# Kernel optimization log

Measured on AMD Instinct MI355X. Metric: run time of the kernel, lower is better.

The kernel has to match this reference:

```python
import jax, jax.numpy as jnp
import numpy as np

N = 4096
D_IN = 1024
D_OUT = 1024
NUM_HEADS = 16
HEAD_DIM = D_OUT // NUM_HEADS


def setup_inputs() -> dict:
    key = jax.random.key(0)
    ks = jax.random.split(key, 7)
    scale = 1.0 / np.sqrt(D_IN)
    return {
        "q": jax.random.normal(ks[0], (N, D_IN), dtype=jnp.float32),
        "k": jax.random.normal(ks[1], (N, D_IN), dtype=jnp.float32),
        "v": jax.random.normal(ks[2], (N, D_IN), dtype=jnp.float32),
        "W_q": jax.random.normal(ks[3], (D_IN, D_OUT), dtype=jnp.float32) * scale,
        "W_k": jax.random.normal(ks[4], (D_IN, D_OUT), dtype=jnp.float32) * scale,
        "W_v": jax.random.normal(ks[5], (D_IN, D_OUT), dtype=jnp.float32) * scale,
        "W_o": jax.random.normal(ks[6], (D_OUT, D_OUT), dtype=jnp.float32) * scale,
    }


def reference(q, k, v, W_q, W_k, W_v, W_o):
    n = q.shape[0]
    # QKV projections -> [h, n, d]
    Q = (q @ W_q).reshape(n, NUM_HEADS, HEAD_DIM).transpose(1, 0, 2)
    K = (k @ W_k).reshape(n, NUM_HEADS, HEAD_DIM).transpose(1, 0, 2)
    V = (v @ W_v).reshape(n, NUM_HEADS, HEAD_DIM).transpose(1, 0, 2)
    scores = jnp.einsum('hid,hjd->hij', Q, K) / jnp.sqrt(jnp.float32(HEAD_DIM))
    attn = jax.nn.softmax(scores, axis=-1)  # dropout p=0.0 (eval) -> no-op
    h = jnp.einsum('hij,hjd->hid', attn, V)
    h = h.transpose(1, 0, 2).reshape(n, D_OUT)
    return h @ W_o
```

## Files before the change

kernel.cpp:

```cpp
#include <hip/hip_runtime.h>
#include <math.h>

#define NTOK   4096
#define DMODEL 1024
#define NHEADS 16
#define HDIM   64
#define KDIM   1024

typedef __attribute__((ext_vector_type(8))) short          bf16x8;
typedef __attribute__((ext_vector_type(4))) float          f32x4;
typedef __attribute__((ext_vector_type(4))) unsigned short us4;

static __device__ __forceinline__ unsigned short f2bf(float f) {
    unsigned int u = __float_as_uint(f);
    u += 0x7fffu + ((u >> 16) & 1u);
    return (unsigned short)(u >> 16);
}

static __device__ __forceinline__ unsigned int pk2bf(float a, float b) {
#if __has_builtin(__builtin_amdgcn_cvt_pk_bf16_f32)
    return __builtin_bit_cast(unsigned int,
                              __builtin_amdgcn_cvt_pk_bf16_f32(a, b));
#else
    unsigned int ua = __float_as_uint(a) + 0x8000u;
    unsigned int ub = __float_as_uint(b) + 0x8000u;
    return __builtin_amdgcn_perm(ub, ua, 0x07060302u);
#endif
}

#if __has_builtin(__builtin_amdgcn_exp2f)
#define EXP2(x) __builtin_amdgcn_exp2f(x)
#else
#define EXP2(x) exp2f(x)
#endif

static __device__ __forceinline__ void async_copy16(void* lds, const void* g) {
    __builtin_amdgcn_global_load_lds(
        (const __attribute__((address_space(1))) unsigned int*)g,
        (__attribute__((address_space(3))) unsigned int*)lds, 16, 0, 0);
}

__global__ __launch_bounds__(256)
void cast_wt_kernel(const float* __restrict__ Wq, const float* __restrict__ Wk,
                    const float* __restrict__ Wv, const float* __restrict__ Wo,
                    unsigned short* __restrict__ Tq, unsigned short* __restrict__ Tk,
                    unsigned short* __restrict__ Tv, unsigned short* __restrict__ To) {
    __shared__ float Ws[64][65];
    const float* W;
    unsigned short* T;
    switch (blockIdx.z) {
        case 0:  W = Wq; T = Tq; break;
        case 1:  W = Wk; T = Tk; break;
        case 2:  W = Wv; T = Tv; break;
        default: W = Wo; T = To; break;
    }
    const int k0 = blockIdx.x * 64, n0 = blockIdx.y * 64;
    const int t = threadIdx.x;
    #pragma unroll
    for (int i = 0; i < 4; i++) {
        int c  = i * 256 + t;
        int kk = c >> 4;
        int n4 = (c & 15) << 2;
        *(float4*)(&Ws[kk][n4]) =
            *(const float4*)(W + (size_t)(k0 + kk) * DMODEL + n0 + n4);
    }
    __syncthreads();
    #pragma unroll
    for (int i = 0; i < 4; i++) {
        int c  = i * 256 + t;
        int nn = c >> 4;
        int k4 = (c & 15) << 2;
        us4 o = { f2bf(Ws[k4 + 0][nn]), f2bf(Ws[k4 + 1][nn]),
                  f2bf(Ws[k4 + 2][nn]), f2bf(Ws[k4 + 3][nn]) };
        *(us4*)(T + (size_t)(n0 + nn) * KDIM + k0 + k4) = o;
    }
}

__global__ __launch_bounds__(256)
void cast_in_kernel(const float* __restrict__ q, const float* __restrict__ k,
                    const float* __restrict__ v,
                    unsigned short* __restrict__ Qb,
                    unsigned short* __restrict__ Kb,
                    unsigned short* __restrict__ Vb) {
    const float* src;
    unsigned short* dst;
    switch (blockIdx.y) {
        case 0:  src = q; dst = Qb; break;
        case 1:  src = k; dst = Kb; break;
        default: src = v; dst = Vb; break;
    }
    size_t i = ((size_t)blockIdx.x * 256 + threadIdx.x) * 8;
    float4 f0 = *(const float4*)(src + i);
    float4 f1 = *(const float4*)(src + i + 4);
    uint2 o0 = { pk2bf(f0.x, f0.y), pk2bf(f0.z, f0.w) };
    uint2 o1 = { pk2bf(f1.x, f1.y), pk2bf(f1.z, f1.w) };
    *(uint2*)(dst + i)     = o0;
    *(uint2*)(dst + i + 4) = o1;
}

__global__ __launch_bounds__(256, 3)
void qkv_gemm_pre(const unsigned short* __restrict__ Qb,
                  const unsigned short* __restrict__ Kb,
                  const unsigned short* __restrict__ Vb,
                  const unsigned short* __restrict__ Btq,
                  const unsigned short* __restrict__ Btk,
                  const unsigned short* __restrict__ Btv,
                  unsigned short* __restrict__ Oq, unsigned short* __restrict__ Ok,
                  unsigned short* __restrict__ Ov) {
    __shared__ unsigned short As[128 * 64];
    __shared__ unsigned short Bs[128 * 64];

    const unsigned short* A;
    const unsigned short* Bt;
    unsigned short* Out;
    int mode;
    float sc;
    switch (blockIdx.z) {
        case 0:  A = Qb; Bt = Btq; Out = Oq; mode = 1; sc = 0.18033688011112042f; break;
        case 1:  A = Kb; Bt = Btk; Out = Ok; mode = 1; sc = 1.0f; break;
        default: A = Vb; Bt = Btv; Out = Ov; mode = 2; sc = 1.0f; break;
    }

    const int t    = threadIdx.x;
    const int w    = t >> 6;
    const int lane = t & 63;
    const int quad = lane >> 4;
    const int l15  = lane & 15;
    const int wr   = w >> 1, wc = w & 1;
    const int bm   = blockIdx.y * 128, bn = blockIdx.x * 128;

    f32x4 acc[4][4];
    #pragma unroll
    for (int i = 0; i < 4; i++)
        #pragma unroll
        for (int j = 0; j < 4; j++) acc[i][j] = (f32x4)(0.f);

    for (int k0 = 0; k0 < KDIM; k0 += 64) {
        __syncthreads();
        #pragma unroll
        for (int i = 0; i < 4; i++) {
            int cb = (i * 4 + w) * 64;
            int c  = cb + lane;
            int r  = c >> 3;
            int ko = (c & 7) * 8;
            async_copy16((void*)(Bs + cb * 8),
                         (const void*)(Bt + (size_t)(bn + r) * KDIM + k0 + ko));
            async_copy16((void*)(As + cb * 8),
                         (const void*)(A + (size_t)(bm + r) * KDIM + k0 + ko));
        }
        __syncthreads();
        #pragma unroll
        for (int kq = 0; kq < 2; kq++) {
            bf16x8 af[4], bf[4];
            #pragma unroll
            for (int mt = 0; mt < 4; mt++)
                af[mt] = *(bf16x8*)(As + (wr * 64 + mt * 16 + l15) * 64 + kq * 32 + quad * 8);
            #pragma unroll
            for (int nt = 0; nt < 4; nt++)
                bf[nt] = *(bf16x8*)(Bs + (wc * 64 + nt * 16 + l15) * 64 + kq * 32 + quad * 8);
            #pragma unroll
            for (int mt = 0; mt < 4; mt++)
                #pragma unroll
                for (int nt = 0; nt < 4; nt++)
                    acc[mt][nt] = __builtin_amdgcn_mfma_f32_16x16x32_bf16(
                        af[mt], bf[nt], acc[mt][nt], 0, 0, 0);
        }
    }

    #pragma unroll
    for (int mt = 0; mt < 4; mt++) {
        #pragma unroll
        for (int nt = 0; nt < 4; nt++) {
            int col  = bn + wc * 64 + nt * 16 + l15;
            int row0 = bm + wr * 64 + mt * 16 + quad * 4;
            if (mode == 1) {
                size_t base = ((size_t)(col >> 6)) * NTOK * HDIM + (col & 63);
                #pragma unroll
                for (int r = 0; r < 4; r++)
                    Out[base + (size_t)(row0 + r) * HDIM] = f2bf(acc[mt][nt][r] * sc);
            } else {
                size_t base = ((size_t)(col >> 6)) * HDIM * NTOK +
                              (size_t)(col & 63) * NTOK + row0;
                us4 o = { f2bf(acc[mt][nt][0]), f2bf(acc[mt][nt][1]),
                          f2bf(acc[mt][nt][2]), f2bf(acc[mt][nt][3]) };
                *(us4*)(Out + base) = o;
            }
        }
    }
}

__global__ __launch_bounds__(256, 3)
void qkv_gemm(const float* __restrict__ Aq, const float* __restrict__ Ak,
              const float* __restrict__ Av,
              const unsigned short* __restrict__ Btq,
              const unsigned short* __restrict__ Btk,
              const unsigned short* __restrict__ Btv,
              unsigned short* __restrict__ Oq, unsigned short* __restrict__ Ok,
              unsigned short* __restrict__ Ov) {
    __shared__ unsigned short As[128 * 64];
    __shared__ unsigned short Bs[128 * 64];

    const float* A;
    const unsigned short* Bt;
    unsigned short* Out;
    int mode;
    float sc;
    switch (blockIdx.z) {
        case 0:  A = Aq; Bt = Btq; Out = Oq; mode = 1; sc = 0.18033688011112042f; break;
        case 1:  A = Ak; Bt = Btk; Out = Ok; mode = 1; sc = 1.0f; break;
        default: A = Av; Bt = Btv; Out = Ov; mode = 2; sc = 1.0f; break;
    }

    const int t    = threadIdx.x;
    const int w    = t >> 6;
    const int lane = t & 63;
    const int quad = lane >> 4;
    const int l15  = lane & 15;
    const int wr   = w >> 1, wc = w & 1;
    const int bm   = blockIdx.y * 128, bn = blockIdx.x * 128;

    f32x4 acc[4][4];
    #pragma unroll
    for (int i = 0; i < 4; i++)
        #pragma unroll
        for (int j = 0; j < 4; j++) acc[i][j] = (f32x4)(0.f);

    for (int k0 = 0; k0 < KDIM; k0 += 64) {
        __syncthreads();
        #pragma unroll
        for (int i = 0; i < 4; i++) {
            int cb = (i * 4 + w) * 64;
            int c  = cb + lane;
            int r  = c >> 3;
            int ko = (c & 7) * 8;
            async_copy16((void*)(Bs + cb * 8),
                         (const void*)(Bt + (size_t)(bn + r) * KDIM + k0 + ko));
        }
        #pragma unroll
        for (int i = 0; i < 4; i++) {
            int c2 = i * 256 + t;
            int r  = c2 >> 3;
            int k8 = (c2 & 7) * 8;
            const float* src = A + (size_t)(bm + r) * KDIM + k0 + k8;
            float4 f0 = *(const float4*)(src);
            float4 f1 = *(const float4*)(src + 4);
            uint2 p0 = { pk2bf(f0.x, f0.y), pk2bf(f0.z, f0.w) };
            uint2 p1 = { pk2bf(f1.x, f1.y), pk2bf(f1.z, f1.w) };
            *(uint2*)(As + r * 64 + k8)     = p0;
            *(uint2*)(As + r * 64 + k8 + 4) = p1;
        }
        __syncthreads();
        #pragma unroll
        for (int kq = 0; kq < 2; kq++) {
            bf16x8 af[4], bf[4];
            #pragma unroll
            for (int mt = 0; mt < 4; mt++)
                af[mt] = *(bf16x8*)(As + (wr * 64 + mt * 16 + l15) * 64 + kq * 32 + quad * 8);
            #pragma unroll
            for (int nt = 0; nt < 4; nt++)
                bf[nt] = *(bf16x8*)(Bs + (wc * 64 + nt * 16 + l15) * 64 + kq * 32 + quad * 8);
            #pragma unroll
            for (int mt = 0; mt < 4; mt++)
                #pragma unroll
                for (int nt = 0; nt < 4; nt++)
                    acc[mt][nt] = __builtin_amdgcn_mfma_f32_16x16x32_bf16(
                        af[mt], bf[nt], acc[mt][nt], 0, 0, 0);
        }
    }

    #pragma unroll
    for (int mt = 0; mt < 4; mt++) {
        #pragma unroll
        for (int nt = 0; nt < 4; nt++) {
            int col  = bn + wc * 64 + nt * 16 + l15;
            int row0 = bm + wr * 64 + mt * 16 + quad * 4;
            if (mode == 1) {
                size_t base = ((size_t)(col >> 6)) * NTOK * HDIM + (col & 63);
                #pragma unroll
                for (int r = 0; r < 4; r++)
                    Out[base + (size_t)(row0 + r) * HDIM] = f2bf(acc[mt][nt][r] * sc);
            } else {
                size_t base = ((size_t)(col >> 6)) * HDIM * NTOK +
                              (size_t)(col & 63) * NTOK + row0;
                us4 o = { f2bf(acc[mt][nt][0]), f2bf(acc[mt][nt][1]),
                          f2bf(acc[mt][nt][2]), f2bf(acc[mt][nt][3]) };
                *(us4*)(Out + base) = o;
            }
        }
    }
}

__global__ __launch_bounds__(256, 3)
void out_gemm(const unsigned short* __restrict__ A,
              const unsigned short* __restrict__ Bt,
              float* __restrict__ Out) {
    __shared__ unsigned short As[64 * 64];
    __shared__ unsigned short Bs[128 * 64];

    const int t    = threadIdx.x;
    const int w    = t >> 6;
    const int lane = t & 63;
    const int quad = lane >> 4;
    const int l15  = lane & 15;
    const int wr   = w >> 1, wc = w & 1;
    const int bm   = blockIdx.y * 64, bn = blockIdx.x * 128;

    f32x4 acc[2][4];
    #pragma unroll
    for (int i = 0; i < 2; i++)
        #pragma unroll
        for (int j = 0; j < 4; j++) acc[i][j] = (f32x4)(0.f);

    for (int k0 = 0; k0 < KDIM; k0 += 64) {
        __syncthreads();
        #pragma unroll
        for (int i = 0; i < 4; i++) {
            int cb = (i * 4 + w) * 64;
            int c  = cb + lane;
            int r  = c >> 3;
            int ko = (c & 7) * 8;
            async_copy16((void*)(Bs + cb * 8),
                         (const void*)(Bt + (size_t)(bn + r) * KDIM + k0 + ko));
        }
        #pragma unroll
        for (int i = 0; i < 2; i++) {
            int cb = (i * 4 + w) * 64;
            int c  = cb + lane;
            int r  = c >> 3;
            int ko = (c & 7) * 8;
            async_copy16((void*)(As + cb * 8),
                         (const void*)(A + (size_t)(bm + r) * KDIM + k0 + ko));
        }
        __syncthreads();
        #pragma unroll
        for (int kq = 0; kq < 2; kq++) {
            bf16x8 af[2], bf[4];
            #pragma unroll
            for (int mt = 0; mt < 2; mt++)
                af[mt] = *(bf16x8*)(As + (wr * 32 + mt * 16 + l15) * 64 + kq * 32 + quad * 8);
            #pragma unroll
            for (int nt = 0; nt < 4; nt++)
                bf[nt] = *(bf16x8*)(Bs + (wc * 64 + nt * 16 + l15) * 64 + kq * 32 + quad * 8);
            #pragma unroll
            for (int mt = 0; mt < 2; mt++)
                #pragma unroll
                for (int nt = 0; nt < 4; nt++)
                    acc[mt][nt] = __builtin_amdgcn_mfma_f32_16x16x32_bf16(
                        af[mt], bf[nt], acc[mt][nt], 0, 0, 0);
        }
    }

    #pragma unroll
    for (int mt = 0; mt < 2; mt++) {
        #pragma unroll
        for (int nt = 0; nt < 4; nt++) {
            int col  = bn + wc * 64 + nt * 16 + l15;
            int row0 = bm + wr * 32 + mt * 16 + quad * 4;
            #pragma unroll
            for (int r = 0; r < 4; r++)
                Out[(size_t)(row0 + r) * DMODEL + col] = acc[mt][nt][r];
        }
    }
}

__global__ __launch_bounds__(256, 4)
void attn_split(const unsigned short* __restrict__ Q,
                const unsigned short* __restrict__ K,
                const unsigned short* __restrict__ Vt,
                unsigned short* __restrict__ PO,
                float* __restrict__ lbuf) {
    __shared__ __align__(16) unsigned short Ks[4096];
    __shared__ __align__(16) unsigned short Vs[4096];
    __shared__ __align__(16) unsigned short Ps[4][16][72];

    const int qt   = blockIdx.x;
    const int h    = blockIdx.y;
    const int half = blockIdx.z;
    const int t    = threadIdx.x;
    const int w    = t >> 6;
    const int lane = t & 63;
    const int quad = lane >> 4;
    const int l15  = lane & 15;

    const unsigned short* Qg =
        Q + ((size_t)h * NTOK + qt * 128 + w * 32 + l15) * HDIM;
    bf16x8 qf[2][2];
    qf[0][0] = *(const bf16x8*)(Qg + quad * 8);
    qf[0][1] = *(const bf16x8*)(Qg + 32 + quad * 8);
    qf[1][0] = *(const bf16x8*)(Qg + 16 * HDIM + quad * 8);
    qf[1][1] = *(const bf16x8*)(Qg + 16 * HDIM + 32 + quad * 8);

    const unsigned short* Kg = K  + ((size_t)h * NTOK + half * 2048) * HDIM;
    const unsigned short* Vg = Vt + (size_t)h * HDIM * NTOK + half * 2048;

    const int rr = t >> 3;
    const int oo = ((t & 7) ^ (rr & 7)) * 8;
    const unsigned short* kbase = Kg + (size_t)rr * HDIM + oo;
    const unsigned short* vbase = Vg + (size_t)rr * NTOK + oo;
    unsigned short* ksd = Ks + w * 512;
    unsigned short* vsd = Vs + w * 512;

    const int xb = l15 & 7;
    const int a0 = l15 * 64 + ((quad    ) ^ xb) * 8;
    const int a1 = l15 * 64 + ((quad + 4) ^ xb) * 8;

    const bf16x8 ones = { 16256, 16256, 16256, 16256,
                          16256, 16256, 16256, 16256 };

    f32x4 O[2][4];
    f32x4 lacc[2];
    #pragma unroll
    for (int tl = 0; tl < 2; tl++) {
        lacc[tl] = (f32x4)(0.f);
        #pragma unroll
        for (int dt = 0; dt < 4; dt++) O[tl][dt] = (f32x4)(0.f);
    }

    for (int kt = 0; kt < 32; kt++) {
        __syncthreads();
        {
            const unsigned short* kp = kbase + (size_t)kt * 64 * HDIM;
            const unsigned short* vp = vbase + kt * 64;
            async_copy16((void*)(ksd),        (const void*)kp);
            async_copy16((void*)(ksd + 2048), (const void*)(kp + 32 * HDIM));
            async_copy16((void*)(vsd),        (const void*)vp);
            async_copy16((void*)(vsd + 2048), (const void*)(vp + (size_t)32 * NTOK));
        }
        __syncthreads();

        f32x4 s[2][4];
        #pragma unroll
        for (int kc = 0; kc < 4; kc++) {
            bf16x8 kf0 = *(bf16x8*)(Ks + kc * 1024 + a0);
            bf16x8 kf1 = *(bf16x8*)(Ks + kc * 1024 + a1);
            #pragma unroll
            for (int tl = 0; tl < 2; tl++) {
                f32x4 acc = (f32x4)(0.f);
                acc = __builtin_amdgcn_mfma_f32_16x16x32_bf16(kf0, qf[tl][0], acc, 0, 0, 0);
                acc = __builtin_amdgcn_mfma_f32_16x16x32_bf16(kf1, qf[tl][1], acc, 0, 0, 0);
                s[tl][kc] = acc;
            }
        }

        bf16x8 vf[4][2];
        #pragma unroll
        for (int dt = 0; dt < 4; dt++) {
            vf[dt][0] = *(bf16x8*)(Vs + dt * 1024 + a0);
            vf[dt][1] = *(bf16x8*)(Vs + dt * 1024 + a1);
        }

        #pragma unroll
        for (int tl = 0; tl < 2; tl++) {
            #pragma unroll
            for (int kc = 0; kc < 4; kc++) {
                float e0 = EXP2(s[tl][kc][0]);
                float e1 = EXP2(s[tl][kc][1]);
                float e2 = EXP2(s[tl][kc][2]);
                float e3 = EXP2(s[tl][kc][3]);
                uint2 p = { pk2bf(e0, e1), pk2bf(e2, e3) };
                *(uint2*)(&Ps[w][l15][kc * 16 + quad * 4]) = p;
            }
            asm volatile("s_waitcnt lgkmcnt(0)" ::: "memory");

            bf16x8 pf0 = *(bf16x8*)(&Ps[w][l15][quad * 8]);
            bf16x8 pf1 = *(bf16x8*)(&Ps[w][l15][32 + quad * 8]);
            lacc[tl] = __builtin_amdgcn_mfma_f32_16x16x32_bf16(ones, pf0, lacc[tl], 0, 0, 0);
            lacc[tl] = __builtin_amdgcn_mfma_f32_16x16x32_bf16(ones, pf1, lacc[tl], 0, 0, 0);
            #pragma unroll
            for (int dt = 0; dt < 4; dt++) {
                O[tl][dt] = __builtin_amdgcn_mfma_f32_16x16x32_bf16(vf[dt][0], pf0, O[tl][dt], 0, 0, 0);
                O[tl][dt] = __builtin_amdgcn_mfma_f32_16x16x32_bf16(vf[dt][1], pf1, O[tl][dt], 0, 0, 0);
            }
        }
    }

    unsigned short* POh = PO + (size_t)half * NTOK * DMODEL;
    #pragma unroll
    for (int tl = 0; tl < 2; tl++) {
        size_t row = (size_t)qt * 128 + w * 32 + tl * 16 + l15;
        #pragma unroll
        for (int dt = 0; dt < 4; dt++) {
            uint2 o = { pk2bf(O[tl][dt][0], O[tl][dt][1]),
                        pk2bf(O[tl][dt][2], O[tl][dt][3]) };
            *(uint2*)(POh + row * DMODEL + h * HDIM + dt * 16 + quad * 4) = o;
        }
        if (quad == 0)
            lbuf[((size_t)half * NHEADS + h) * NTOK + row] = lacc[tl][0];
    }
}

__global__ __launch_bounds__(256)
void combine_kernel(const unsigned short* __restrict__ PO,
                    const float* __restrict__ lbuf,
                    unsigned short* __restrict__ ctx) {
    size_t idx = ((size_t)blockIdx.x * 256 + threadIdx.x) * 8;
    int row = (int)(idx >> 10);
    int c   = (int)(idx & 1023);
    int h   = c >> 6;
    uint4 a = *(const uint4*)(PO + idx);
    uint4 b = *(const uint4*)(PO + (size_t)NTOK * DMODEL + idx);
    float la = lbuf[(size_t)h * NTOK + row];
    float lb = lbuf[(size_t)NHEADS * NTOK + (size_t)h * NTOK + row];
    float inv = 1.f / (la + lb);
    auto comb = [&](unsigned int x, unsigned int y) -> unsigned int {
        float x0 = __uint_as_float(x << 16);
        float x1 = __uint_as_float(x & 0xffff0000u);
        float y0 = __uint_as_float(y << 16);
        float y1 = __uint_as_float(y & 0xffff0000u);
        return pk2bf((x0 + y0) * inv, (x1 + y1) * inv);
    };
    uint4 o = { comb(a.x, b.x), comb(a.y, b.y), comb(a.z, b.z), comb(a.w, b.w) };
    *(uint4*)(ctx + idx) = o;
}

__global__ __launch_bounds__(256)
void attn_mfma(const unsigned short* __restrict__ Q,
               const unsigned short* __restrict__ K,
               const unsigned short* __restrict__ Vt,
               unsigned short* __restrict__ ctx) {
    __shared__ __align__(16) unsigned short Ks[2 * 4096];
    __shared__ __align__(16) unsigned short Vs[2 * 4096];
    __shared__ __align__(16) unsigned short Ps[4][32][72];

    const int h    = blockIdx.y;
    const int qt   = blockIdx.x;
    const int t    = threadIdx.x;
    const int w    = t >> 6;
    const int lane = t & 63;
    const int quad = lane >> 4;
    const int l15  = lane & 15;

    const unsigned short* Qg =
        Q + ((size_t)h * NTOK + qt * 128 + w * 32 + l15) * HDIM;
    bf16x8 qf[2][2];
    qf[0][0] = *(const bf16x8*)(Qg + quad * 8);
    qf[0][1] = *(const bf16x8*)(Qg + 32 + quad * 8);
    qf[1][0] = *(const bf16x8*)(Qg + 16 * HDIM + quad * 8);
    qf[1][1] = *(const bf16x8*)(Qg + 16 * HDIM + 32 + quad * 8);

    const unsigned short* Kg = K  + (size_t)h * NTOK * HDIM;
    const unsigned short* Vg = Vt + (size_t)h * HDIM * NTOK;

    const int rr = t >> 3;
    const int oo = ((t & 7) ^ (rr & 7)) * 8;
    const unsigned short* kbase = Kg + (size_t)rr * HDIM + oo;
    const unsigned short* vbase = Vg + (size_t)rr * NTOK + oo;
    unsigned short* ksd = Ks + w * 512;
    unsigned short* vsd = Vs + w * 512;

    auto stage = [&](int kt, int b) {
        const unsigned short* kp = kbase + (size_t)kt * 64 * HDIM;
        const unsigned short* vp = vbase + kt * 64;
        async_copy16((void*)(ksd + b * 4096),        (const void*)kp);
        async_copy16((void*)(ksd + b * 4096 + 2048), (const void*)(kp + 32 * HDIM));
        async_copy16((void*)(vsd + b * 4096),        (const void*)vp);
        async_copy16((void*)(vsd + b * 4096 + 2048), (const void*)(vp + (size_t)32 * NTOK));
    };

    const int xb = l15 & 7;
    const int a0 = l15 * 64 + ((quad    ) ^ xb) * 8;
    const int a1 = l15 * 64 + ((quad + 4) ^ xb) * 8;

    const bf16x8 ones = { 16256, 16256, 16256, 16256,
                          16256, 16256, 16256, 16256 };

    f32x4 O[2][4];
    f32x4 lacc[2];
    #pragma unroll
    for (int tl = 0; tl < 2; tl++) {
        lacc[tl] = (f32x4)(0.f);
        #pragma unroll
        for (int dt = 0; dt < 4; dt++) O[tl][dt] = (f32x4)(0.f);
    }

    stage(0, 0);

    for (int kt = 0; kt < NTOK / 64; kt++) {
        const int cur = kt & 1;
        __syncthreads();
        if (kt + 1 < NTOK / 64) stage(kt + 1, cur ^ 1);

        f32x4 s[2][4];
        #pragma unroll
        for (int kc = 0; kc < 4; kc++) {
            bf16x8 kf0 = *(bf16x8*)(Ks + cur * 4096 + kc * 1024 + a0);
            bf16x8 kf1 = *(bf16x8*)(Ks + cur * 4096 + kc * 1024 + a1);
            #pragma unroll
            for (int tl = 0; tl < 2; tl++) {
                f32x4 acc = (f32x4)(0.f);
                acc = __builtin_amdgcn_mfma_f32_16x16x32_bf16(kf0, qf[tl][0], acc, 0, 0, 0);
                acc = __builtin_amdgcn_mfma_f32_16x16x32_bf16(kf1, qf[tl][1], acc, 0, 0, 0);
                s[tl][kc] = acc;
            }
        }

        bf16x8 vf[4][2];
        #pragma unroll
        for (int dt = 0; dt < 4; dt++) {
            vf[dt][0] = *(bf16x8*)(Vs + cur * 4096 + dt * 1024 + a0);
            vf[dt][1] = *(bf16x8*)(Vs + cur * 4096 + dt * 1024 + a1);
        }

        #pragma unroll
        for (int tl = 0; tl < 2; tl++) {
            #pragma unroll
            for (int kc = 0; kc < 4; kc++) {
                float e0 = EXP2(s[tl][kc][0]);
                float e1 = EXP2(s[tl][kc][1]);
                float e2 = EXP2(s[tl][kc][2]);
                float e3 = EXP2(s[tl][kc][3]);
                uint2 p = { pk2bf(e0, e1), pk2bf(e2, e3) };
                *(uint2*)(&Ps[w][tl * 16 + l15][kc * 16 + quad * 4]) = p;
            }
            asm volatile("s_waitcnt lgkmcnt(0)" ::: "memory");

            bf16x8 pf0 = *(bf16x8*)(&Ps[w][tl * 16 + l15][quad * 8]);
            bf16x8 pf1 = *(bf16x8*)(&Ps[w][tl * 16 + l15][32 + quad * 8]);
            lacc[tl] = __builtin_amdgcn_mfma_f32_16x16x32_bf16(ones, pf0, lacc[tl], 0, 0, 0);
            lacc[tl] = __builtin_amdgcn_mfma_f32_16x16x32_bf16(ones, pf1, lacc[tl], 0, 0, 0);
            #pragma unroll
            for (int dt = 0; dt < 4; dt++) {
                O[tl][dt] = __builtin_amdgcn_mfma_f32_16x16x32_bf16(vf[dt][0], pf0, O[tl][dt], 0, 0, 0);
                O[tl][dt] = __builtin_amdgcn_mfma_f32_16x16x32_bf16(vf[dt][1], pf1, O[tl][dt], 0, 0, 0);
            }
        }
    }

    #pragma unroll
    for (int tl = 0; tl < 2; tl++) {
        float inv = 1.f / lacc[tl][0];
        size_t row = (size_t)qt * 128 + w * 32 + tl * 16 + l15;
        #pragma unroll
        for (int dt = 0; dt < 4; dt++) {
            uint2 o = { pk2bf(O[tl][dt][0] * inv, O[tl][dt][1] * inv),
                        pk2bf(O[tl][dt][2] * inv, O[tl][dt][3] * inv) };
            *(uint2*)(ctx + row * DMODEL + h * HDIM + dt * 16 + quad * 4) = o;
        }
    }
}

extern "C" void kernel_launch(void* const* d_in, const int* in_sizes, int n_in,
                              void* d_out, int out_size, void* d_ws, size_t ws_size,
                              hipStream_t stream) {
    const float* q  = (const float*)d_in[0];
    const float* k  = (const float*)d_in[1];
    const float* v  = (const float*)d_in[2];
    const float* Wq = (const float*)d_in[3];
    const float* Wk = (const float*)d_in[4];
    const float* Wv = (const float*)d_in[5];
    const float* Wo = (const float*)d_in[6];
    float* out = (float*)d_out;

    unsigned short* WqT = (unsigned short*)d_ws;
    unsigned short* WkT = WqT + (size_t)DMODEL * KDIM;
    unsigned short* WvT = WkT + (size_t)DMODEL * KDIM;
    unsigned short* WoT = WvT + (size_t)DMODEL * KDIM;
    unsigned short* Qh  = WoT + (size_t)DMODEL * KDIM;
    unsigned short* Kh  = Qh  + (size_t)NTOK * DMODEL;
    unsigned short* Vth = Kh  + (size_t)NTOK * DMODEL;
    unsigned short* ctx = Vth + (size_t)NTOK * DMODEL;
    unsigned short* Qb  = ctx + (size_t)NTOK * DMODEL;
    unsigned short* Kb  = Qb  + (size_t)NTOK * DMODEL;
    unsigned short* Vb  = Kb  + (size_t)NTOK * DMODEL;
    unsigned short* PO  = Qb;
    float*          lb  = (float*)(PO + (size_t)2 * NTOK * DMODEL);

    const bool bigws = ws_size >= (size_t)67108864;

    cast_wt_kernel<<<dim3(16, 16, 4), 256, 0, stream>>>(Wq, Wk, Wv, Wo,
                                                        WqT, WkT, WvT, WoT);
    if (bigws) {
        cast_in_kernel<<<dim3(2048, 3), 256, 0, stream>>>(q, k, v, Qb, Kb, Vb);
        qkv_gemm_pre<<<dim3(DMODEL / 128, NTOK / 128, 3), 256, 0, stream>>>(
            Qb, Kb, Vb, WqT, WkT, WvT, Qh, Kh, Vth);
        attn_split<<<dim3(NTOK / 128, NHEADS, 2), 256, 0, stream>>>(
            Qh, Kh, Vth, PO, lb);
        combine_kernel<<<dim3(NTOK * DMODEL / 8 / 256), 256, 0, stream>>>(
            PO, lb, ctx);
    } else {
        qkv_gemm<<<dim3(DMODEL / 128, NTOK / 128, 3), 256, 0, stream>>>(
            q, k, v, WqT, WkT, WvT, Qh, Kh, Vth);
        attn_mfma<<<dim3(NTOK / 128, NHEADS), 256, 0, stream>>>(Qh, Kh, Vth, ctx);
    }
    out_gemm<<<dim3(DMODEL / 128, NTOK / 64), 256, 0, stream>>>(ctx, WoT, out);
}
```

Baseline: 256.2 us.

## Rewrite attention inner loop with 32x32 MFMA, register-resident P, double-buffered K/V

Switches the attention kernel from 16x16x32 to 32x32x16 bf16 MFMAs, keeping the probability tile in registers by exchanging halves with v_permlane32_swap instead of a round trip through shared memory. Row sums are accumulated with scalar adds instead of MFMA against a ones vector. K/V tiles are double-buffered so the next tile's async copy overlaps with compute, which removes one barrier per iteration. Shared memory per block roughly doubles for K/V, which may reduce occupancy, and the new permlane-based fragment layout must line up with the swizzle.

New measurement: 259.3 us. Within noise of the previous version (+1.2%).

```diff
diff --git a/kernel.cpp b/kernel.cpp
--- a/kernel.cpp
+++ b/kernel.cpp
@@ -9,6 +9,8 @@
 
 typedef __attribute__((ext_vector_type(8))) short          bf16x8;
 typedef __attribute__((ext_vector_type(4))) float          f32x4;
+typedef __attribute__((ext_vector_type(16))) float         f32x16;
+typedef __attribute__((ext_vector_type(4))) unsigned int   u32x4;
 typedef __attribute__((ext_vector_type(4))) unsigned short us4;
 
 static __device__ __forceinline__ unsigned short f2bf(float f) {
@@ -369,9 +371,8 @@
                 const unsigned short* __restrict__ Vt,
                 unsigned short* __restrict__ PO,
                 float* __restrict__ lbuf) {
-    __shared__ __align__(16) unsigned short Ks[4096];
-    __shared__ __align__(16) unsigned short Vs[4096];
-    __shared__ __align__(16) unsigned short Ps[4][16][72];
+    __shared__ __align__(16) unsigned short Ks[2 * 4096];
+    __shared__ __align__(16) unsigned short Vs[2 * 4096];
 
     const int qt   = blockIdx.x;
     const int h    = blockIdx.y;
@@ -379,16 +380,16 @@
     const int t    = threadIdx.x;
     const int w    = t >> 6;
     const int lane = t & 63;
-    const int quad = lane >> 4;
-    const int l15  = lane & 15;
+    const int r    = lane & 31;
+    const int hi   = lane >> 5;
+    const int xh   = (r & 7) ^ hi;
 
     const unsigned short* Qg =
-        Q + ((size_t)h * NTOK + qt * 128 + w * 32 + l15) * HDIM;
-    bf16x8 qf[2][2];
-    qf[0][0] = *(const bf16x8*)(Qg + quad * 8);
-    qf[0][1] = *(const bf16x8*)(Qg + 32 + quad * 8);
-    qf[1][0] = *(const bf16x8*)(Qg + 16 * HDIM + quad * 8);
-    qf[1][1] = *(const bf16x8*)(Qg + 16 * HDIM + 32 + quad * 8);
+        Q + ((size_t)h * NTOK + qt * 128 + w * 32 + r) * HDIM + hi * 8;
+    bf16x8 qf[4];
+    #pragma unroll
+    for (int ds = 0; ds < 4; ds++)
+        qf[ds] = *(const bf16x8*)(Qg + ds * 16);
 
     const unsigned short* Kg = K  + ((size_t)h * NTOK + half * 2048) * HDIM;
     const unsigned short* Vg = Vt + (size_t)h * HDIM * NTOK + half * 2048;
@@ -400,93 +401,92 @@
     unsigned short* ksd = Ks + w * 512;
     unsigned short* vsd = Vs + w * 512;
 
-    const int xb = l15 & 7;
-    const int a0 = l15 * 64 + ((quad    ) ^ xb) * 8;
-    const int a1 = l15 * 64 + ((quad + 4) ^ xb) * 8;
-
-    const bf16x8 ones = { 16256, 16256, 16256, 16256,
-                          16256, 16256, 16256, 16256 };
-
-    f32x4 O[2][4];
-    f32x4 lacc[2];
-    #pragma unroll
-    for (int tl = 0; tl < 2; tl++) {
-        lacc[tl] = (f32x4)(0.f);
-        #pragma unroll
-        for (int dt = 0; dt < 4; dt++) O[tl][dt] = (f32x4)(0.f);
-    }
+    auto stage = [&](int kt, int b) {
+        const unsigned short* kp = kbase + (size_t)kt * 64 * HDIM;
+        const unsigned short* vp = vbase + kt * 64;
+        async_copy16((void*)(ksd + b * 4096),        (const void*)kp);
+        async_copy16((void*)(ksd + b * 4096 + 2048), (const void*)(kp + 32 * HDIM));
+        async_copy16((void*)(vsd + b * 4096),        (const void*)vp);
+        async_copy16((void*)(vsd + b * 4096 + 2048), (const void*)(vp + (size_t)32 * NTOK));
+    };
+
+    f32x16 O0 = (f32x16)(0.f), O1 = (f32x16)(0.f);
+    float l0 = 0.f, l1 = 0.f, l2 = 0.f, l3 = 0.f;
+
+    stage(0, 0);
 
     for (int kt = 0; kt < 32; kt++) {
-        __syncthreads();
-        {
-            const unsigned short* kp = kbase + (size_t)kt * 64 * HDIM;
-            const unsigned short* vp = vbase + kt * 64;
-            async_copy16((void*)(ksd),        (const void*)kp);
-            async_copy16((void*)(ksd + 2048), (const void*)(kp + 32 * HDIM));
-            async_copy16((void*)(vsd),        (const void*)vp);
-            async_copy16((void*)(vsd + 2048), (const void*)(vp + (size_t)32 * NTOK));
-        }
-        __syncthreads();
-
-        f32x4 s[2][4];
-        #pragma unroll
-        for (int kc = 0; kc < 4; kc++) {
-            bf16x8 kf0 = *(bf16x8*)(Ks + kc * 1024 + a0);
-            bf16x8 kf1 = *(bf16x8*)(Ks + kc * 1024 + a1);
-            #pragma unroll
-            for (int tl = 0; tl < 2; tl++) {
-                f32x4 acc = (f32x4)(0.f);
-                acc = __builtin_amdgcn_mfma_f32_16x16x32_bf16(kf0, qf[tl][0], acc, 0, 0, 0);
-                acc = __builtin_amdgcn_mfma_f32_16x16x32_bf16(kf1, qf[tl][1], acc, 0, 0, 0);
-                s[tl][kc] = acc;
+        const int cur = kt & 1;
+        __syncthreads();
+        if (kt + 1 < 32) stage(kt + 1, cur ^ 1);
+
+        const unsigned short* Kb = Ks + cur * 4096 + r * 64;
+        const unsigned short* Vb = Vs + cur * 4096 + r * 64;
+
+        f32x16 S0 = (f32x16)(0.f), S1 = (f32x16)(0.f);
+        #pragma unroll
+        for (int ds = 0; ds < 4; ds++) {
+            int c = ((2 * ds) ^ xh) * 8;
+            bf16x8 k0 = *(const bf16x8*)(Kb + c);
+            bf16x8 k1 = *(const bf16x8*)(Kb + 2048 + c);
+            S0 = __builtin_amdgcn_mfma_f32_32x32x16_bf16(k0, qf[ds], S0, 0, 0, 0);
+            S1 = __builtin_amdgcn_mfma_f32_32x32x16_bf16(k1, qf[ds], S1, 0, 0, 0);
+        }
+
+        #pragma unroll
+        for (int kb = 0; kb < 2; kb++) {
+            const f32x16 S = kb ? S1 : S0;
+            float p[16];
+            #pragma unroll
+            for (int i = 0; i < 16; i++) p[i] = EXP2(S[i]);
+            #pragma unroll
+            for (int i = 0; i < 4; i++) {
+                l0 += p[i * 4 + 0];
+                l1 += p[i * 4 + 1];
+                l2 += p[i * 4 + 2];
+                l3 += p[i * 4 + 3];
             }
-        }
-
-        bf16x8 vf[4][2];
-        #pragma unroll
-        for (int dt = 0; dt < 4; dt++) {
-            vf[dt][0] = *(bf16x8*)(Vs + dt * 1024 + a0);
-            vf[dt][1] = *(bf16x8*)(Vs + dt * 1024 + a1);
-        }
-
-        #pragma unroll
-        for (int tl = 0; tl < 2; tl++) {
-            #pragma unroll
-            for (int kc = 0; kc < 4; kc++) {
-                float e0 = EXP2(s[tl][kc][0]);
-                float e1 = EXP2(s[tl][kc][1]);
-                float e2 = EXP2(s[tl][kc][2]);
-                float e3 = EXP2(s[tl][kc][3]);
-                uint2 p = { pk2bf(e0, e1), pk2bf(e2, e3) };
-                *(uint2*)(&Ps[w][l15][kc * 16 + quad * 4]) = p;
+            #pragma unroll
+            for (int g = 0; g < 2; g++) {
+                unsigned int w0 = pk2bf(p[g * 8 + 0], p[g * 8 + 1]);
+                unsigned int w2 = pk2bf(p[g * 8 + 4], p[g * 8 + 5]);
+                unsigned int w1 = pk2bf(p[g * 8 + 2], p[g * 8 + 3]);
+                unsigned int w3 = pk2bf(p[g * 8 + 6], p[g * 8 + 7]);
+                asm volatile("v_permlane32_swap_b32 %0, %1"
+                             : "+v"(w0), "+v"(w2));
+                asm volatile("v_permlane32_swap_b32 %0, %1"
+                             : "+v"(w1), "+v"(w3));
+                u32x4 pw = { w0, w1, w2, w3 };
+                bf16x8 pf = __builtin_bit_cast(bf16x8, pw);
+                int kg = kb * 2 + g;
+                int c  = ((2 * kg) ^ xh) * 8;
+                bf16x8 v0 = *(const bf16x8*)(Vb + c);
+                bf16x8 v1 = *(const bf16x8*)(Vb + 2048 + c);
+                O0 = __builtin_amdgcn_mfma_f32_32x32x16_bf16(v0, pf, O0, 0, 0, 0);
+                O1 = __builtin_amdgcn_mfma_f32_32x32x16_bf16(v1, pf, O1, 0, 0, 0);
             }
-            asm volatile("s_waitcnt lgkmcnt(0)" ::: "memory");
-
-            bf16x8 pf0 = *(bf16x8*)(&Ps[w][l15][quad * 8]);
-            bf16x8 pf1 = *(bf16x8*)(&Ps[w][l15][32 + quad * 8]);
-            lacc[tl] = __builtin_amdgcn_mfma_f32_16x16x32_bf16(ones, pf0, lacc[tl], 0, 0, 0);
-            lacc[tl] = __builtin_amdgcn_mfma_f32_16x16x32_bf16(ones, pf1, lacc[tl], 0, 0, 0);
-            #pragma unroll
-            for (int dt = 0; dt < 4; dt++) {
-                O[tl][dt] = __builtin_amdgcn_mfma_f32_16x16x32_bf16(vf[dt][0], pf0, O[tl][dt], 0, 0, 0);
-                O[tl][dt] = __builtin_amdgcn_mfma_f32_16x16x32_bf16(vf[dt][1], pf1, O[tl][dt], 0, 0, 0);
-            }
-        }
-    }
+        }
+    }
+
+    float lt  = (l0 + l1) + (l2 + l3);
+    float ltot = lt + __shfl_xor(lt, 32, 64);
 
     unsigned short* POh = PO + (size_t)half * NTOK * DMODEL;
-    #pragma unroll
-    for (int tl = 0; tl < 2; tl++) {
-        size_t row = (size_t)qt * 128 + w * 32 + tl * 16 + l15;
-        #pragma unroll
-        for (int dt = 0; dt < 4; dt++) {
-            uint2 o = { pk2bf(O[tl][dt][0], O[tl][dt][1]),
-                        pk2bf(O[tl][dt][2], O[tl][dt][3]) };
-            *(uint2*)(POh + row * DMODEL + h * HDIM + dt * 16 + quad * 4) = o;
-        }
-        if (quad == 0)
-            lbuf[((size_t)half * NHEADS + h) * NTOK + row] = lacc[tl][0];
-    }
+    size_t row = (size_t)qt * 128 + w * 32 + r;
+    unsigned short* dst = POh + row * DMODEL + h * HDIM;
+    #pragma unroll
+    for (int db = 0; db < 2; db++) {
+        const f32x16 O = db ? O1 : O0;
+        #pragma unroll
+        for (int g = 0; g < 4; g++) {
+            int d = db * 32 + g * 8 + hi * 4;
+            uint2 o = { pk2bf(O[g * 4 + 0], O[g * 4 + 1]),
+                        pk2bf(O[g * 4 + 2], O[g * 4 + 3]) };
+            *(uint2*)(dst + d) = o;
+        }
+    }
+    if (hi == 0)
+        lbuf[((size_t)half * NHEADS + h) * NTOK + row] = ltot;
 }
 
 __global__ __launch_bounds__(256)
```
